# Kernel tuning notes

Measured on AMD Instinct MI355X. Metric: run time of the kernel, lower is better.

Reference implementation:

```python
import jax, jax.numpy as jnp
import numpy as np

B, T, F, H = 4096, 48, 64, 128


def _uniform(key, shape, stdv):
    return jax.random.uniform(key, shape, jnp.float32, -stdv, stdv)


def setup_inputs() -> dict:
    key = jax.random.key(0)
    ks = jax.random.split(key, 24)
    values = jax.random.normal(ks[0], (B, T, F), jnp.float32)
    masks = (jax.random.uniform(ks[1], (B, T, F)) < 0.8).astype(jnp.float32)
    deltas = jax.random.uniform(ks[2], (B, T, F), jnp.float32)
    sH = 1.0 / np.sqrt(H)
    sF = 1.0 / np.sqrt(F)
    inp = {
        "values": values, "masks": masks, "deltas": deltas,
        # TemporalDecay h: W [H, F], b [H] (stdv = 1/sqrt(out=H))
        "Wdh": _uniform(ks[3], (H, F), sH), "bdh": _uniform(ks[4], (H,), sH),
        # TemporalDecay x (diag): W [F, F], b [F]
        "Wdx": _uniform(ks[5], (F, F), sF), "bdx": _uniform(ks[6], (F,), sF),
        # hist_reg: Linear(H -> F)
        "Wh": _uniform(ks[7], (F, H), sH), "bh": _uniform(ks[8], (F,), sH),
        # feat_reg: masked F x F
        "Wf": _uniform(ks[9], (F, F), sF), "bf": _uniform(ks[10], (F,), sF),
        # weight_combine: Linear(2F -> F)
        "Wc": _uniform(ks[11], (F, 2 * F), 1.0 / np.sqrt(2 * F)),
        "bc": _uniform(ks[12], (F,), 1.0 / np.sqrt(2 * F)),
        # LSTMCell(2F -> H): gates in PyTorch order i, f, g, o
        "W_ih": _uniform(ks[13], (4 * H, 2 * F), sH),
        "W_hh": _uniform(ks[14], (4 * H, H), sH),
        "b_ih": _uniform(ks[15], (4 * H,), sH),
        "b_hh": _uniform(ks[16], (4 * H,), sH),
        # out: Linear(H -> 1)
        "Wo": _uniform(ks[17], (1, H), sH), "bo": _uniform(ks[18], (1,), sH),
    }
    return inp


def reference(values, masks, deltas, Wdh, bdh, Wdx, bdx, Wh, bh, Wf, bf,
              Wc, bc, W_ih, W_hh, b_ih, b_hh, Wo, bo):
    impute_weight = 1.0
    b, t, f = values.shape
    h_dim = Wdh.shape[0]
    eye = jnp.eye(f, dtype=values.dtype)
    Wdx_m = Wdx * eye            # diagonal temporal decay
    Wf_m = Wf * (1.0 - eye)

    def step(carry, xt):
        h, c, loss = carry
        x, m, d = xt  # each [B, F]
        gamma_h = jnp.exp(-jax.nn.relu(d @ Wdh.T + bdh))        # [B, H]
        gamma_x = jnp.exp(-jax.nn.relu(d @ Wdx_m.T + bdx))      # [B, F]
        h = h * gamma_h
        x_h = h @ Wh.T + bh
        denom = jnp.sum(m) + 1e-5
        loss = loss + jnp.sum(jnp.abs(x - x_h) * m) / denom
        x_c = m * x + (1.0 - m) * x_h
        z_h = x_c @ Wf_m.T + bf
        loss = loss + jnp.sum(jnp.abs(x - z_h) * m) / denom
        alpha = jnp.concatenate([gamma_x, m], axis=1) @ Wc.T + bc
        c_h = alpha * z_h + (1.0 - alpha) * x_h
        loss = loss + jnp.sum(jnp.abs(x - c_h) * m) / denom
        c_c = m * x + (1.0 - m) * c_h
        inputs = jnp.concatenate([c_c, m], axis=1)  # [B, 2F]
        gates = inputs @ W_ih.T + b_ih + h @ W_hh.T + b_hh
        i_g, f_g, g_g, o_g = jnp.split(gates, 4, axis=1)
        c = jax.nn.sigmoid(f_g) * c + jax.nn.sigmoid(i_g) * jnp.tanh(g_g)
        h = jax.nn.sigmoid(o_g) * jnp.tanh(c)
        return (h, c, loss), c_c

    init = (jnp.zeros((b, h_dim), values.dtype),
            jnp.zeros((b, h_dim), values.dtype),
            jnp.zeros((), values.dtype))
    xs = (jnp.swapaxes(values, 0, 1),
          jnp.swapaxes(masks, 0, 1),
          jnp.swapaxes(deltas, 0, 1))
    (h, c, x_loss), imps = jax.lax.scan(step, init, xs)
    imputations = jnp.swapaxes(imps, 0, 1)  # [B, T, F]
    predictions = h @ Wo.T + bo             # [B, 1]
    return x_loss * impute_weight, imputations, predictions
```

## Files before the change

kernel.cpp:

```cpp
#include <hip/hip_runtime.h>
#include <hip/hip_bf16.h>
#include <math.h>

#define BB 4096
#define TT 48
#define FF 64
#define HH 128
#define ROWS 16
#define NT 512
#define NBLK (BB / ROWS)

typedef __attribute__((ext_vector_type(8))) short short8;
typedef __attribute__((ext_vector_type(4))) float f32x4;

__device__ __forceinline__ float sigm(float x) { return 1.f / (1.f + __expf(-x)); }
__device__ __forceinline__ float tanh_f(float x) { return 2.f / (1.f + __expf(-2.f * x)) - 1.f; }

__global__ __launch_bounds__(256) void prep_kernel(
    const float* __restrict__ W_ih, const float* __restrict__ W_hh,
    const float* __restrict__ Wdh,  const float* __restrict__ Wh,
    const float* __restrict__ Wf,   const float* __restrict__ Wc,
    __hip_bfloat16* __restrict__ frags) {
    const int idx = blockIdx.x * 256 + threadIdx.x;
    float v;
    if (idx < 131072) {
        const int jj = idx & 7;
        const int lane = (idx >> 3) & 63;
        const int ks = (idx >> 9) & 7;
        const int tile = idx >> 12;
        const int n = tile * 16 + (lane & 15);
        const int k = ks * 32 + ((lane >> 4) << 3) + jj;
        v = (k < 128) ? W_ih[n * 128 + k] : W_hh[n * 128 + (k - 128)];
    } else {
        const int u = idx - 131072;
        const int jj = u & 7;
        const int lane = (u >> 3) & 63;
        const int lq = lane & 15, q8 = (lane >> 4) << 3;
        if (u < 8192) {
            const int ks = (u >> 9) & 1, nt = u >> 10;
            const int n = nt * 16 + lq, k = ks * 32 + q8 + jj;
            v = Wdh[n * 64 + k];
        } else if (u < 16384) {
            const int uu = u - 8192;
            const int ks = (uu >> 9) & 3, nt = uu >> 11;
            const int n = nt * 16 + lq, k = ks * 32 + q8 + jj;
            v = Wh[n * 128 + k];
        } else if (u < 20480) {
            const int uu = u - 16384;
            const int ks = (uu >> 9) & 1, nt = uu >> 10;
            const int n = nt * 16 + lq, k = ks * 32 + q8 + jj;
            v = (k == n) ? 0.f : Wf[n * 64 + k];
        } else {
            const int uu = u - 20480;
            const int ks = (uu >> 9) & 3, nt = uu >> 11;
            const int n = nt * 16 + lq, k = ks * 32 + q8 + jj;
            v = Wc[n * 128 + k];
        }
    }
    frags[idx] = __float2bfloat16(v);
}

__global__ __launch_bounds__(NT, 2) void rits_kernel(
    const float* __restrict__ values, const float* __restrict__ masks,
    const float* __restrict__ deltas,
    const float* __restrict__ Wdx, const float* __restrict__ bdx,
    const float* __restrict__ bdh, const float* __restrict__ bh,
    const float* __restrict__ bf,  const float* __restrict__ bc,
    const float* __restrict__ b_ih, const float* __restrict__ b_hh,
    const float* __restrict__ Wo,  const float* __restrict__ bo,
    const __hip_bfloat16* __restrict__ frags,
    float* __restrict__ ws_msum,
    float* __restrict__ ws_numer,
    float* __restrict__ out_imp, float* __restrict__ out_pred)
{
    __shared__ __hip_bfloat16 dbuf[ROWS][72];
    __shared__ __hip_bfloat16 xcbuf[ROWS][72];
    __shared__ __hip_bfloat16 hbuf[ROWS][136];
    __shared__ __hip_bfloat16 gxm[ROWS][136];
    __shared__ __hip_bfloat16 ccm[ROWS][136];
    __shared__ float x_lds[ROWS][65];
    __shared__ float m_lds[ROWS][65];
    __shared__ float redm[8];
    __shared__ float redl[8];

    const int tid = threadIdx.x;
    const int bid = blockIdx.x;
    const int b0 = bid * ROWS;
    const int lane = tid & 63;
    const int wv = tid >> 6;
    const int quad = lane >> 4;
    const int lq = lane & 15;

    for (int i = tid; i < ROWS * 136; i += NT) ((unsigned short*)hbuf)[i] = 0;

    const float wdx_l = Wdx[lane * (FF + 1)];
    const float bdx_l = bdx[lane];

    const int j_ln = wv * 16 + lq;
    const float bdh_j = bdh[j_ln];
    const float bI = b_ih[j_ln]       + b_hh[j_ln];
    const float bF = b_ih[128 + j_ln] + b_hh[128 + j_ln];
    const float bG = b_ih[256 + j_ln] + b_hh[256 + j_ln];
    const float bO = b_ih[384 + j_ln] + b_hh[384 + j_ln];

    const int f46 = (wv & 3) * 16 + lq;
    const float bh_f = bh[f46];
    const float bf_f = bf[f46];
    const float bc_f = bc[f46];

    const short8* f8 = (const short8*)frags;

    float c_reg[4];
    #pragma unroll
    for (int r = 0; r < 4; ++r) c_reg[r] = 0.f;

    __syncthreads();

    for (int t = 0; t < TT; ++t) {
        float msum_th = 0.f;
        #pragma unroll
        for (int q = 0; q < 2; ++q) {
            const int r = wv + 8 * q;
            const int off = ((b0 + r) * TT + t) * FF + lane;
            const float xv = values[off], mv = masks[off], dv = deltas[off];
            x_lds[r][lane] = xv;
            m_lds[r][lane] = mv;
            msum_th += mv;
            dbuf[r][lane] = __float2bfloat16(dv);
            const float gx = __expf(-fmaxf(fmaf(dv, wdx_l, bdx_l), 0.f));
            gxm[r][lane] = __float2bfloat16(gx);
            const __hip_bfloat16 mb = __float2bfloat16(mv);
            gxm[r][64 + lane] = mb;
            ccm[r][64 + lane] = mb;
        }
        #pragma unroll
        for (int off = 32; off; off >>= 1) msum_th += __shfl_down(msum_th, off, 64);
        if (lane == 0) redm[wv] = msum_th;
        __syncthreads();
        if (tid == 0) {
            float s = 0.f;
            #pragma unroll
            for (int w = 0; w < 8; ++w) s += redm[w];
            ws_msum[t * NBLK + bid] = s;
        }

        {
            f32x4 acc = {0.f, 0.f, 0.f, 0.f};
            #pragma unroll
            for (int ks = 0; ks < 2; ++ks) {
                const short8 a = *(const short8*)&dbuf[lq][ks * 32 + quad * 8];
                const short8 b = f8[16384 + ((wv * 2 + ks) << 6) + lane];
                acc = __builtin_amdgcn_mfma_f32_16x16x32_bf16(a, b, acc, 0, 0, 0);
            }
            #pragma unroll
            for (int r = 0; r < 4; ++r) {
                const int row = quad * 4 + r;
                const float gh = __expf(-fmaxf(acc[r] + bdh_j, 0.f));
                const float hd = __bfloat162float(hbuf[row][j_ln]) * gh;
                hbuf[row][j_ln] = __float2bfloat16(hd);
            }
        }
        __syncthreads();

        float xv_r[4], mv_r[4], xh_r[4];
        float stepsum = 0.f;

        if (wv < 4) {
            f32x4 acc = {0.f, 0.f, 0.f, 0.f};
            #pragma unroll
            for (int ks = 0; ks < 4; ++ks) {
                const short8 a = *(const short8*)&hbuf[lq][ks * 32 + quad * 8];
                const short8 b = f8[17408 + ((wv * 4 + ks) << 6) + lane];
                acc = __builtin_amdgcn_mfma_f32_16x16x32_bf16(a, b, acc, 0, 0, 0);
            }
            #pragma unroll
            for (int r = 0; r < 4; ++r) {
                const int row = quad * 4 + r;
                const float xh = acc[r] + bh_f;
                xh_r[r] = xh;
                const float xv = x_lds[row][f46], mv = m_lds[row][f46];
                xv_r[r] = xv; mv_r[r] = mv;
                stepsum += mv * fabsf(xv - xh);
                xcbuf[row][f46] = __float2bfloat16(fmaf(mv, xv, (1.f - mv) * xh));
            }
        }
        __syncthreads();

        if (wv < 4) {
            f32x4 acc5 = {0.f, 0.f, 0.f, 0.f};
            #pragma unroll
            for (int ks = 0; ks < 2; ++ks) {
                const short8 a = *(const short8*)&xcbuf[lq][ks * 32 + quad * 8];
                const short8 b = f8[18432 + ((wv * 2 + ks) << 6) + lane];
                acc5 = __builtin_amdgcn_mfma_f32_16x16x32_bf16(a, b, acc5, 0, 0, 0);
            }
            f32x4 acc6 = {0.f, 0.f, 0.f, 0.f};
            #pragma unroll
            for (int ks = 0; ks < 4; ++ks) {
                const short8 a = *(const short8*)&gxm[lq][ks * 32 + quad * 8];
                const short8 b = f8[18944 + ((wv * 4 + ks) << 6) + lane];
                acc6 = __builtin_amdgcn_mfma_f32_16x16x32_bf16(a, b, acc6, 0, 0, 0);
            }
            #pragma unroll
            for (int r = 0; r < 4; ++r) {
                const int row = quad * 4 + r;
                const float zh = acc5[r] + bf_f;
                stepsum += mv_r[r] * fabsf(xv_r[r] - zh);
                const float alpha = acc6[r] + bc_f;
                const float ch = fmaf(alpha, zh, (1.f - alpha) * xh_r[r]);
                stepsum += mv_r[r] * fabsf(xv_r[r] - ch);
                const float cc = fmaf(mv_r[r], xv_r[r], (1.f - mv_r[r]) * ch);
                ccm[row][f46] = __float2bfloat16(cc);
                out_imp[((b0 + row) * TT + t) * FF + f46] = cc;
            }
        }
        #pragma unroll
        for (int off = 32; off; off >>= 1) stepsum += __shfl_down(stepsum, off, 64);
        if (lane == 0) redl[wv] = stepsum;
        __syncthreads();
        if (tid == 0) {
            float s = 0.f;
            #pragma unroll
            for (int w = 0; w < 8; ++w) s += redl[w];
            ws_numer[t * NBLK + bid] = s;
        }

        {
            f32x4 acc[4];
            #pragma unroll
            for (int g = 0; g < 4; ++g) acc[g] = (f32x4){0.f, 0.f, 0.f, 0.f};
            #pragma unroll
            for (int ks = 0; ks < 8; ++ks) {
                const short8 a = (ks < 4)
                    ? *(const short8*)&ccm[lq][ks * 32 + quad * 8]
                    : *(const short8*)&hbuf[lq][(ks - 4) * 32 + quad * 8];
                #pragma unroll
                for (int g = 0; g < 4; ++g) {
                    const short8 b = f8[(((g * 8 + wv) * 8 + ks) << 6) + lane];
                    acc[g] = __builtin_amdgcn_mfma_f32_16x16x32_bf16(a, b, acc[g], 0, 0, 0);
                }
            }
            float hnew[4];
            #pragma unroll
            for (int r = 0; r < 4; ++r) {
                const float ig = sigm(acc[0][r] + bI);
                const float fg = sigm(acc[1][r] + bF);
                const float gg = tanh_f(acc[2][r] + bG);
                const float og = sigm(acc[3][r] + bO);
                c_reg[r] = fmaf(fg, c_reg[r], ig * gg);
                hnew[r] = og * tanh_f(c_reg[r]);
            }
            __syncthreads();
            #pragma unroll
            for (int r = 0; r < 4; ++r)
                hbuf[quad * 4 + r][j_ln] = __float2bfloat16(hnew[r]);
        }
        __syncthreads();
    }

    {
        const int r = tid >> 5, l = tid & 31;
        float s = 0.f;
        #pragma unroll
        for (int k = l; k < HH; k += 32) s += __bfloat162float(hbuf[r][k]) * Wo[k];
        #pragma unroll
        for (int off = 16; off; off >>= 1) s += __shfl_down(s, off, 32);
        if (l == 0) out_pred[b0 + r] = s + bo[0];
    }
}

__global__ __launch_bounds__(256) void final_kernel(const float* __restrict__ ws_msum,
                                                    const float* __restrict__ ws_numer,
                                                    float* __restrict__ out_loss) {
    const int tid = threadIdx.x;
    const int lane = tid & 63, wv = tid >> 6;
    __shared__ float red[4];
    float acc = 0.f;
    for (int t = wv; t < TT; t += 4) {
        float ms = 0.f, ns = 0.f;
        #pragma unroll
        for (int c = 0; c < NBLK / 64; ++c) {
            ms += ws_msum[t * NBLK + c * 64 + lane];
            ns += ws_numer[t * NBLK + c * 64 + lane];
        }
        #pragma unroll
        for (int off = 32; off; off >>= 1) {
            ms += __shfl_down(ms, off, 64);
            ns += __shfl_down(ns, off, 64);
        }
        if (lane == 0) acc += ns / (ms + 1e-5f);
    }
    if (lane == 0) red[wv] = acc;
    __syncthreads();
    if (tid == 0) out_loss[0] = red[0] + red[1] + red[2] + red[3];
}

extern "C" void kernel_launch(void* const* d_in, const int* in_sizes, int n_in,
                              void* d_out, int out_size, void* d_ws, size_t ws_size,
                              hipStream_t stream) {
    const float* values = (const float*)d_in[0];
    const float* masks  = (const float*)d_in[1];
    const float* deltas = (const float*)d_in[2];
    const float* Wdh  = (const float*)d_in[3];
    const float* bdh  = (const float*)d_in[4];
    const float* Wdx  = (const float*)d_in[5];
    const float* bdx  = (const float*)d_in[6];
    const float* Wh   = (const float*)d_in[7];
    const float* bh   = (const float*)d_in[8];
    const float* Wf   = (const float*)d_in[9];
    const float* bf   = (const float*)d_in[10];
    const float* Wc   = (const float*)d_in[11];
    const float* bc   = (const float*)d_in[12];
    const float* W_ih = (const float*)d_in[13];
    const float* W_hh = (const float*)d_in[14];
    const float* b_ih = (const float*)d_in[15];
    const float* b_hh = (const float*)d_in[16];
    const float* Wo   = (const float*)d_in[17];
    const float* bo   = (const float*)d_in[18];

    __hip_bfloat16* frags = (__hip_bfloat16*)d_ws;
    float* ws_msum  = (float*)((char*)d_ws + 320 * 1024);
    float* ws_numer = ws_msum + TT * NBLK;

    float* out_loss = (float*)d_out;
    float* out_imp  = out_loss + 1;
    float* out_pred = out_imp + (size_t)BB * TT * FF;

    prep_kernel<<<624, 256, 0, stream>>>(W_ih, W_hh, Wdh, Wh, Wf, Wc, frags);
    rits_kernel<<<NBLK, NT, 0, stream>>>(
        values, masks, deltas, Wdx, bdx, bdh, bh, bf, bc,
        b_ih, b_hh, Wo, bo, frags, ws_msum, ws_numer, out_imp, out_pred);
    final_kernel<<<1, 256, 0, stream>>>(ws_msum, ws_numer, out_loss);
}
```

Before: 385.5 us.

## Precompute loss denominators, prefetch next step, double-buffer h, cut per-step barriers

Per-timestep mask sums now come from separate reduction kernels that produce an inverse denominator. This lets the recurrent kernel scale its loss locally and reduce it once at the end, instead of doing block reductions and barriers every step. The next timestep's inputs are loaded from global memory ahead of time and staged into LDS during the LSTM phase. The hidden state is double-buffered so the decayed h and the new h no longer need an extra barrier. The alpha matmul moves to waves 0-3 while waves 4-7 compute the decay, which balances the first phase. The cost is two extra small launches and one extra read of the masks array.

```diff
diff --git a/kernel.cpp b/kernel.cpp
--- a/kernel.cpp
+++ b/kernel.cpp
@@ -60,6 +60,39 @@
     frags[idx] = __float2bfloat16(v);
 }
 
+__global__ __launch_bounds__(256) void denom1_kernel(const float* __restrict__ masks,
+                                                     float* __restrict__ partials) {
+    const int t = blockIdx.x >> 5;
+    const int s = blockIdx.x & 31;
+    const int tid = threadIdx.x;
+    float acc = 0.f;
+    #pragma unroll
+    for (int k = 0; k < 8; ++k) {
+        const int i = k * 256 + tid;
+        const int b = s * 128 + (i >> 4);
+        const int f = (i & 15) << 2;
+        const float4 v = *(const float4*)&masks[((size_t)b * TT + t) * FF + f];
+        acc += v.x + v.y + v.z + v.w;
+    }
+    #pragma unroll
+    for (int off = 32; off; off >>= 1) acc += __shfl_down(acc, off, 64);
+    __shared__ float red[4];
+    if ((tid & 63) == 0) red[tid >> 6] = acc;
+    __syncthreads();
+    if (tid == 0) partials[blockIdx.x] = red[0] + red[1] + red[2] + red[3];
+}
+
+__global__ __launch_bounds__(64) void denom2_kernel(const float* __restrict__ partials,
+                                                    float* __restrict__ inv_denom) {
+    const int t = threadIdx.x;
+    if (t < TT) {
+        float s = 0.f;
+        #pragma unroll
+        for (int i = 0; i < 32; ++i) s += partials[t * 32 + i];
+        inv_denom[t] = 1.f / (s + 1e-5f);
+    }
+}
+
 __global__ __launch_bounds__(NT, 2) void rits_kernel(
     const float* __restrict__ values, const float* __restrict__ masks,
     const float* __restrict__ deltas,
@@ -69,18 +102,18 @@
     const float* __restrict__ b_ih, const float* __restrict__ b_hh,
     const float* __restrict__ Wo,  const float* __restrict__ bo,
     const __hip_bfloat16* __restrict__ frags,
-    float* __restrict__ ws_msum,
-    float* __restrict__ ws_numer,
+    const float* __restrict__ inv_denom,
+    float* __restrict__ ws_lossblk,
     float* __restrict__ out_imp, float* __restrict__ out_pred)
 {
     __shared__ __hip_bfloat16 dbuf[ROWS][72];
     __shared__ __hip_bfloat16 xcbuf[ROWS][72];
-    __shared__ __hip_bfloat16 hbuf[ROWS][136];
+    __shared__ __hip_bfloat16 hbufA[ROWS][136];
+    __shared__ __hip_bfloat16 hbufB[ROWS][136];
     __shared__ __hip_bfloat16 gxm[ROWS][136];
     __shared__ __hip_bfloat16 ccm[ROWS][136];
     __shared__ float x_lds[ROWS][65];
     __shared__ float m_lds[ROWS][65];
-    __shared__ float redm[8];
     __shared__ float redl[8];
 
     const int tid = threadIdx.x;
@@ -91,13 +124,12 @@
     const int quad = lane >> 4;
     const int lq = lane & 15;
 
-    for (int i = tid; i < ROWS * 136; i += NT) ((unsigned short*)hbuf)[i] = 0;
+    for (int i = tid; i < ROWS * 136; i += NT) ((unsigned short*)hbufA)[i] = 0;
 
     const float wdx_l = Wdx[lane * (FF + 1)];
     const float bdx_l = bdx[lane];
 
     const int j_ln = wv * 16 + lq;
-    const float bdh_j = bdh[j_ln];
     const float bI = b_ih[j_ln]       + b_hh[j_ln];
     const float bF = b_ih[128 + j_ln] + b_hh[128 + j_ln];
     const float bG = b_ih[256 + j_ln] + b_hh[256 + j_ln];
@@ -108,68 +140,93 @@
     const float bf_f = bf[f46];
     const float bc_f = bc[f46];
 
+    const float bdh0 = bdh[(wv & 3) * 32 + lq];
+    const float bdh1 = bdh[(wv & 3) * 32 + 16 + lq];
+
     const short8* f8 = (const short8*)frags;
 
     float c_reg[4];
     #pragma unroll
     for (int r = 0; r < 4; ++r) c_reg[r] = 0.f;
-
+    float loss_acc = 0.f;
+
+    float xn[2], mn[2], dn[2];
+    #pragma unroll
+    for (int q = 0; q < 2; ++q) {
+        const int r = wv + 8 * q;
+        const int off = ((b0 + r) * TT + 0) * FF + lane;
+        xn[q] = values[off]; mn[q] = masks[off]; dn[q] = deltas[off];
+    }
+    #pragma unroll
+    for (int q = 0; q < 2; ++q) {
+        const int r = wv + 8 * q;
+        x_lds[r][lane] = xn[q];
+        m_lds[r][lane] = mn[q];
+        dbuf[r][lane] = __float2bfloat16(dn[q]);
+        const float gx = __expf(-fmaxf(fmaf(dn[q], wdx_l, bdx_l), 0.f));
+        gxm[r][lane] = __float2bfloat16(gx);
+        gxm[r][64 + lane] = __float2bfloat16(mn[q]);
+    }
     __syncthreads();
 
     for (int t = 0; t < TT; ++t) {
-        float msum_th = 0.f;
-        #pragma unroll
-        for (int q = 0; q < 2; ++q) {
-            const int r = wv + 8 * q;
-            const int off = ((b0 + r) * TT + t) * FF + lane;
-            const float xv = values[off], mv = masks[off], dv = deltas[off];
-            x_lds[r][lane] = xv;
-            m_lds[r][lane] = mv;
-            msum_th += mv;
-            dbuf[r][lane] = __float2bfloat16(dv);
-            const float gx = __expf(-fmaxf(fmaf(dv, wdx_l, bdx_l), 0.f));
-            gxm[r][lane] = __float2bfloat16(gx);
-            const __hip_bfloat16 mb = __float2bfloat16(mv);
-            gxm[r][64 + lane] = mb;
-            ccm[r][64 + lane] = mb;
-        }
-        #pragma unroll
-        for (int off = 32; off; off >>= 1) msum_th += __shfl_down(msum_th, off, 64);
-        if (lane == 0) redm[wv] = msum_th;
-        __syncthreads();
-        if (tid == 0) {
-            float s = 0.f;
-            #pragma unroll
-            for (int w = 0; w < 8; ++w) s += redm[w];
-            ws_msum[t * NBLK + bid] = s;
-        }
-
+        const float invd = inv_denom[t];
+
+        #pragma unroll
+        for (int q = 0; q < 2; ++q)
+            ccm[wv + 8 * q][64 + lane] = __float2bfloat16(mn[q]);
+
+        float al_r[4];
+        if (wv < 4) {
+            f32x4 acc = {0.f, 0.f, 0.f, 0.f};
+            #pragma unroll
+            for (int ks = 0; ks < 4; ++ks) {
+                const short8 a = *(const short8*)&gxm[lq][ks * 32 + quad * 8];
+                const short8 b = f8[18944 + ((wv * 4 + ks) << 6) + lane];
+                acc = __builtin_amdgcn_mfma_f32_16x16x32_bf16(a, b, acc, 0, 0, 0);
+            }
+            #pragma unroll
+            for (int r = 0; r < 4; ++r) al_r[r] = acc[r] + bc_f;
+        } else {
+            #pragma unroll
+            for (int u = 0; u < 2; ++u) {
+                const int tile = (wv - 4) * 2 + u;
+                f32x4 acc = {0.f, 0.f, 0.f, 0.f};
+                #pragma unroll
+                for (int ks = 0; ks < 2; ++ks) {
+                    const short8 a = *(const short8*)&dbuf[lq][ks * 32 + quad * 8];
+                    const short8 b = f8[16384 + ((tile * 2 + ks) << 6) + lane];
+                    acc = __builtin_amdgcn_mfma_f32_16x16x32_bf16(a, b, acc, 0, 0, 0);
+                }
+                const int col = tile * 16 + lq;
+                const float bdh_c = (u == 0) ? bdh0 : bdh1;
+                #pragma unroll
+                for (int r = 0; r < 4; ++r) {
+                    const int row = quad * 4 + r;
+                    const float gh = __expf(-fmaxf(acc[r] + bdh_c, 0.f));
+                    const float hd = __bfloat162float(hbufA[row][col]) * gh;
+                    hbufB[row][col] = __float2bfloat16(hd);
+                }
+            }
+        }
         {
-            f32x4 acc = {0.f, 0.f, 0.f, 0.f};
-            #pragma unroll
-            for (int ks = 0; ks < 2; ++ks) {
-                const short8 a = *(const short8*)&dbuf[lq][ks * 32 + quad * 8];
-                const short8 b = f8[16384 + ((wv * 2 + ks) << 6) + lane];
-                acc = __builtin_amdgcn_mfma_f32_16x16x32_bf16(a, b, acc, 0, 0, 0);
-            }
-            #pragma unroll
-            for (int r = 0; r < 4; ++r) {
-                const int row = quad * 4 + r;
-                const float gh = __expf(-fmaxf(acc[r] + bdh_j, 0.f));
-                const float hd = __bfloat162float(hbuf[row][j_ln]) * gh;
-                hbuf[row][j_ln] = __float2bfloat16(hd);
+            const int tn = (t < TT - 1) ? t + 1 : t;
+            #pragma unroll
+            for (int q = 0; q < 2; ++q) {
+                const int r = wv + 8 * q;
+                const int off = ((b0 + r) * TT + tn) * FF + lane;
+                xn[q] = values[off]; mn[q] = masks[off]; dn[q] = deltas[off];
             }
         }
         __syncthreads();
 
         float xv_r[4], mv_r[4], xh_r[4];
         float stepsum = 0.f;
-
         if (wv < 4) {
             f32x4 acc = {0.f, 0.f, 0.f, 0.f};
             #pragma unroll
             for (int ks = 0; ks < 4; ++ks) {
-                const short8 a = *(const short8*)&hbuf[lq][ks * 32 + quad * 8];
+                const short8 a = *(const short8*)&hbufB[lq][ks * 32 + quad * 8];
                 const short8 b = f8[17408 + ((wv * 4 + ks) << 6) + lane];
                 acc = __builtin_amdgcn_mfma_f32_16x16x32_bf16(a, b, acc, 0, 0, 0);
             }
@@ -194,19 +251,12 @@
                 const short8 b = f8[18432 + ((wv * 2 + ks) << 6) + lane];
                 acc5 = __builtin_amdgcn_mfma_f32_16x16x32_bf16(a, b, acc5, 0, 0, 0);
             }
-            f32x4 acc6 = {0.f, 0.f, 0.f, 0.f};
-            #pragma unroll
-            for (int ks = 0; ks < 4; ++ks) {
-                const short8 a = *(const short8*)&gxm[lq][ks * 32 + quad * 8];
-                const short8 b = f8[18944 + ((wv * 4 + ks) << 6) + lane];
-                acc6 = __builtin_amdgcn_mfma_f32_16x16x32_bf16(a, b, acc6, 0, 0, 0);
-            }
             #pragma unroll
             for (int r = 0; r < 4; ++r) {
                 const int row = quad * 4 + r;
                 const float zh = acc5[r] + bf_f;
                 stepsum += mv_r[r] * fabsf(xv_r[r] - zh);
-                const float alpha = acc6[r] + bc_f;
+                const float alpha = al_r[r];
                 const float ch = fmaf(alpha, zh, (1.f - alpha) * xh_r[r]);
                 stepsum += mv_r[r] * fabsf(xv_r[r] - ch);
                 const float cc = fmaf(mv_r[r], xv_r[r], (1.f - mv_r[r]) * ch);
@@ -214,16 +264,8 @@
                 out_imp[((b0 + row) * TT + t) * FF + f46] = cc;
             }
         }
-        #pragma unroll
-        for (int off = 32; off; off >>= 1) stepsum += __shfl_down(stepsum, off, 64);
-        if (lane == 0) redl[wv] = stepsum;
+        loss_acc = fmaf(stepsum, invd, loss_acc);
         __syncthreads();
-        if (tid == 0) {
-            float s = 0.f;
-            #pragma unroll
-            for (int w = 0; w < 8; ++w) s += redl[w];
-            ws_numer[t * NBLK + bid] = s;
-        }
 
         {
             f32x4 acc[4];
@@ -233,14 +275,23 @@
             for (int ks = 0; ks < 8; ++ks) {
                 const short8 a = (ks < 4)
                     ? *(const short8*)&ccm[lq][ks * 32 + quad * 8]
-                    : *(const short8*)&hbuf[lq][(ks - 4) * 32 + quad * 8];
+                    : *(const short8*)&hbufB[lq][(ks - 4) * 32 + quad * 8];
                 #pragma unroll
                 for (int g = 0; g < 4; ++g) {
                     const short8 b = f8[(((g * 8 + wv) * 8 + ks) << 6) + lane];
                     acc[g] = __builtin_amdgcn_mfma_f32_16x16x32_bf16(a, b, acc[g], 0, 0, 0);
                 }
             }
-            float hnew[4];
+            #pragma unroll
+            for (int q = 0; q < 2; ++q) {
+                const int r = wv + 8 * q;
+                x_lds[r][lane] = xn[q];
+                m_lds[r][lane] = mn[q];
+                dbuf[r][lane] = __float2bfloat16(dn[q]);
+                const float gx = __expf(-fmaxf(fmaf(dn[q], wdx_l, bdx_l), 0.f));
+                gxm[r][lane] = __float2bfloat16(gx);
+                gxm[r][64 + lane] = __float2bfloat16(mn[q]);
+            }
             #pragma unroll
             for (int r = 0; r < 4; ++r) {
                 const float ig = sigm(acc[0][r] + bI);
@@ -248,12 +299,8 @@
                 const float gg = tanh_f(acc[2][r] + bG);
                 const float og = sigm(acc[3][r] + bO);
                 c_reg[r] = fmaf(fg, c_reg[r], ig * gg);
-                hnew[r] = og * tanh_f(c_reg[r]);
-            }
-            __syncthreads();
-            #pragma unroll
-            for (int r = 0; r < 4; ++r)
-                hbuf[quad * 4 + r][j_ln] = __float2bfloat16(hnew[r]);
+                hbufA[quad * 4 + r][j_ln] = __float2bfloat16(og * tanh_f(c_reg[r]));
+            }
         }
         __syncthreads();
     }
@@ -262,35 +309,31 @@
         const int r = tid >> 5, l = tid & 31;
         float s = 0.f;
         #pragma unroll
-        for (int k = l; k < HH; k += 32) s += __bfloat162float(hbuf[r][k]) * Wo[k];
+        for (int k = l; k < HH; k += 32) s += __bfloat162float(hbufA[r][k]) * Wo[k];
         #pragma unroll
         for (int off = 16; off; off >>= 1) s += __shfl_down(s, off, 32);
         if (l == 0) out_pred[b0 + r] = s + bo[0];
     }
-}
-
-__global__ __launch_bounds__(256) void final_kernel(const float* __restrict__ ws_msum,
-                                                    const float* __restrict__ ws_numer,
+    #pragma unroll
+    for (int off = 32; off; off >>= 1) loss_acc += __shfl_down(loss_acc, off, 64);
+    if (lane == 0) redl[wv] = loss_acc;
+    __syncthreads();
+    if (tid == 0) {
+        float s = 0.f;
+        #pragma unroll
+        for (int w = 0; w < 8; ++w) s += redl[w];
+        ws_lossblk[bid] = s;
+    }
+}
+
+__global__ __launch_bounds__(256) void final_kernel(const float* __restrict__ ws_lossblk,
                                                     float* __restrict__ out_loss) {
     const int tid = threadIdx.x;
-    const int lane = tid & 63, wv = tid >> 6;
+    float s = ws_lossblk[tid];
+    #pragma unroll
+    for (int off = 32; off; off >>= 1) s += __shfl_down(s, off, 64);
     __shared__ float red[4];
-    float acc = 0.f;
-    for (int t = wv; t < TT; t += 4) {
-        float ms = 0.f, ns = 0.f;
-        #pragma unroll
-        for (int c = 0; c < NBLK / 64; ++c) {
-            ms += ws_msum[t * NBLK + c * 64 + lane];
-            ns += ws_numer[t * NBLK + c * 64 + lane];
-        }
-        #pragma unroll
-        for (int off = 32; off; off >>= 1) {
-            ms += __shfl_down(ms, off, 64);
-            ns += __shfl_down(ns, off, 64);
-        }
-        if (lane == 0) acc += ns / (ms + 1e-5f);
-    }
-    if (lane == 0) red[wv] = acc;
+    if ((tid & 63) == 0) red[tid >> 6] = s;
     __syncthreads();
     if (tid == 0) out_loss[0] = red[0] + red[1] + red[2] + red[3];
 }
@@ -319,16 +362,19 @@
     const float* bo   = (const float*)d_in[18];
 
     __hip_bfloat16* frags = (__hip_bfloat16*)d_ws;
-    float* ws_msum  = (float*)((char*)d_ws + 320 * 1024);
-    float* ws_numer = ws_msum + TT * NBLK;
+    float* inv_denom  = (float*)((char*)d_ws + 320 * 1024);
+    float* partials   = inv_denom + 64;
+    float* ws_lossblk = partials + 2048;
 
     float* out_loss = (float*)d_out;
     float* out_imp  = out_loss + 1;
     float* out_pred = out_imp + (size_t)BB * TT * FF;
 
     prep_kernel<<<624, 256, 0, stream>>>(W_ih, W_hh, Wdh, Wh, Wf, Wc, frags);
+    denom1_kernel<<<TT * 32, 256, 0, stream>>>(masks, partials);
+    denom2_kernel<<<1, 64, 0, stream>>>(partials, inv_denom);
     rits_kernel<<<NBLK, NT, 0, stream>>>(
         values, masks, deltas, Wdx, bdx, bdh, bh, bf, bc,
-        b_ih, b_hh, Wo, bo, frags, ws_msum, ws_numer, out_imp, out_pred);
-    final_kernel<<<1, 256, 0, stream>>>(ws_msum, ws_numer, out_loss);
-}
+        b_ih, b_hh, Wo, bo, frags, inv_denom, ws_lossblk, out_imp, out_pred);
+    final_kernel<<<1, 256, 0, stream>>>(ws_lossblk, out_loss);
+}
```

Measured after the change: 357.3 us. 7.3% less time.
